# Kernel optimization log

Hardware: AMD Instinct MI355X
Metric: run time of the kernel (lower is better)

Reference implementation:

```python
import jax, jax.numpy as jnp
import numpy as np

N_NODES = 131072
N_EDGES = 1048576
N_GRAPHS = 1024
EMB = 96
HID = 64
OUT = 3
NEG_SLOPE = 0.2  # PyG GATConv default leaky_relu slope


def setup_inputs() -> dict:
    key = jax.random.key(0)
    ks = jax.random.split(key, 8)
    x = jax.random.normal(ks[0], (N_NODES, EMB), dtype=jnp.float32)
    edge_index = jax.random.randint(ks[1], (2, N_EDGES), 0, N_NODES, dtype=jnp.int64)
    batch = jnp.sort(jax.random.randint(ks[2], (N_NODES,), 0, N_GRAPHS, dtype=jnp.int64))
    s = 1.0 / np.sqrt(EMB)
    W = jax.random.uniform(ks[3], (EMB, HID), jnp.float32, -s, s)       # GATConv lin (no bias)
    att_src = jax.random.uniform(ks[4], (HID,), jnp.float32, -s, s)     # a_src
    att_dst = jax.random.uniform(ks[5], (HID,), jnp.float32, -s, s)     # a_dst
    bias_gat = jnp.zeros((HID,), jnp.float32)
    sf = 1.0 / np.sqrt(HID)
    fc_w = jax.random.uniform(ks[6], (OUT, HID), jnp.float32, -sf, sf)
    fc_b = jax.random.uniform(ks[7], (OUT,), jnp.float32, -sf, sf)
    return {"x": x, "edge_index": edge_index, "batch": batch, "W": W,
            "att_src": att_src, "att_dst": att_dst, "bias_gat": bias_gat,
            "fc_w": fc_w, "fc_b": fc_b}


def _segment_softmax(logits, seg, num_segments):
    # numerically stable softmax over edges grouped by target node
    m = jax.ops.segment_max(logits, seg, num_segments=num_segments)
    e = jnp.exp(logits - m[seg])
    z = jax.ops.segment_sum(e, seg, num_segments=num_segments)
    return e / (z[seg] + 1e-16)


def reference(x, edge_index, batch, W, att_src, att_dst, bias_gat, fc_w, fc_b):
    N = x.shape[0]
    # PyG GATConv (heads=1): add self loops
    loop = jnp.arange(N, dtype=edge_index.dtype)
    src = jnp.concatenate([edge_index[0], loop])
    dst = jnp.concatenate([edge_index[1], loop])

    h = x @ W                                    # [N, HID]
    a_s = h @ att_src                            # [N]
    a_d = h @ att_dst                            # [N]
    logits = jax.nn.leaky_relu(a_s[src] + a_d[dst], NEG_SLOPE)  # [E]
    alpha = _segment_softmax(logits, dst, N)     # softmax over in-edges per target
    out = jax.ops.segment_sum(alpha[:, None] * h[src], dst, num_segments=N)
    out = out + bias_gat                         # [N, HID]

    # global_mean_pool over graphs
    sums = jax.ops.segment_sum(out, batch, num_segments=N_GRAPHS)
    cnt = jax.ops.segment_sum(jnp.ones((N,), out.dtype), batch, num_segments=N_GRAPHS)
    pooled = sums / jnp.maximum(cnt, 1.0)[:, None]  # [G, HID]

    logits_out = pooled @ fc_w.T + fc_b          # [G, OUT]
    return jax.nn.log_softmax(logits_out, axis=1)
```

## Files before the change

### kernel.cpp

```cpp
#include <hip/hip_runtime.h>
#include <hip/hip_fp16.h>

#define N_NODES 131072
#define N_EDGES 1048576
#define N_GRAPHS 1024
#define EMB 96
#define HID 64
#define OUT 3
#define CAP 32
#define NBKT 512
#define NCHUNK 256
#define BCAP 32
#define LCAP 16

typedef _Float16 half8 __attribute__((ext_vector_type(8)));
typedef float float4v __attribute__((ext_vector_type(4)));

__global__ __launch_bounds__(512, 4) void k_front(
    const int* __restrict__ src, const int* __restrict__ dst,
    int* __restrict__ ebuf, int* __restrict__ ccnt,
    const float* __restrict__ x, const float* __restrict__ W,
    const float* __restrict__ att_src, const float* __restrict__ att_dst,
    __half* __restrict__ h, float* __restrict__ a_s, float* __restrict__ a_d,
    float* __restrict__ poolz)
{
    int tid = threadIdx.x;
    __shared__ int smem[NBKT * LCAP + NBKT];

    if (blockIdx.x < NCHUNK) {
        int blk = blockIdx.x;
        int* lists16 = smem;
        int* bcnt = smem + NBKT * LCAP;
        bcnt[tid] = 0;
        if (blk < 33) {
            int idx = blk * 512 + tid;
            if (idx < (N_GRAPHS * HID + N_GRAPHS) / 4)
                ((float4*)poolz)[idx] = (float4){0.f, 0.f, 0.f, 0.f};
        }
        __syncthreads();
        int e0 = blk * 4096;
        #pragma unroll
        for (int i = 0; i < 8; ++i) {
            int e = e0 + i * 512 + tid;
            int sv = src[e], dv = dst[e];
            int b = dv >> 8;
            int packed = (sv << 8) | (dv & 255);
            int r = atomicAdd(&bcnt[b], 1);
            if (r < LCAP)
                lists16[b * LCAP + r] = packed;
            else if (r < BCAP)
                ebuf[((size_t)blk * NBKT + b) * BCAP + r] = packed;
        }
        __syncthreads();
        #pragma unroll
        for (int it = 0; it < 16; ++it) {
            int idx = it * 512 + tid;
            int seg = idx >> 4, s = idx & 15;
            ebuf[((size_t)blk * NBKT + seg) * BCAP + s] = lists16[idx];
        }
        int v = bcnt[tid];
        ccnt[blk * NBKT + tid] = v < BCAP ? v : BCAP;
    } else {
        int sub = blockIdx.x - NCHUNK;
        _Float16* lwt = (_Float16*)smem;
        #pragma unroll
        for (int i = 0; i < 12; ++i) {
            int idx = i * 512 + tid;
            lwt[(idx & 63) * 104 + (idx >> 6)] = (_Float16)W[idx];
        }
        __syncthreads();

        int lane = tid & 63;
        int w = tid >> 6;
        int m16 = lane & 15;
        int quad = lane >> 4;
        int rowbase = sub * 128 + w * 16;

        half8 bf[4][3];
        #pragma unroll
        for (int nt = 0; nt < 4; ++nt)
            #pragma unroll
            for (int kb = 0; kb < 3; ++kb)
                bf[nt][kb] = *(const half8*)(lwt + (nt * 16 + m16) * 104
                                             + kb * 32 + quad * 8);

        float4v acc[4];
        #pragma unroll
        for (int nt = 0; nt < 4; ++nt)
            acc[nt] = (float4v){0.f, 0.f, 0.f, 0.f};

        const float* xrow = x + (size_t)(rowbase + m16) * EMB + quad * 8;
        #pragma unroll
        for (int kb = 0; kb < 3; ++kb) {
            float4 xa = *(const float4*)(xrow + kb * 32);
            float4 xb = *(const float4*)(xrow + kb * 32 + 4);
            half8 af;
            af[0] = (_Float16)xa.x; af[1] = (_Float16)xa.y;
            af[2] = (_Float16)xa.z; af[3] = (_Float16)xa.w;
            af[4] = (_Float16)xb.x; af[5] = (_Float16)xb.y;
            af[6] = (_Float16)xb.z; af[7] = (_Float16)xb.w;
            #pragma unroll
            for (int nt = 0; nt < 4; ++nt)
                acc[nt] = __builtin_amdgcn_mfma_f32_16x16x32_f16(
                    af, bf[nt][kb], acc[nt], 0, 0, 0);
        }

        float asv[4], adv[4];
        #pragma unroll
        for (int nt = 0; nt < 4; ++nt) {
            asv[nt] = att_src[nt * 16 + m16];
            adv[nt] = att_dst[nt * 16 + m16];
        }

        #pragma unroll
        for (int r = 0; r < 4; ++r) {
            int row = rowbase + quad * 4 + r;
            float ps = 0.f, pd = 0.f;
            #pragma unroll
            for (int nt = 0; nt < 4; ++nt) {
                float v = acc[nt][r];
                h[(size_t)row * HID + nt * 16 + m16] = __float2half(v);
                ps += v * asv[nt];
                pd += v * adv[nt];
            }
            #pragma unroll
            for (int off = 8; off >= 1; off >>= 1) {
                ps += __shfl_xor(ps, off, 64);
                pd += __shfl_xor(pd, off, 64);
            }
            if (m16 == 0) { a_s[row] = ps; a_d[row] = pd; }
        }
    }
}

__global__ __launch_bounds__(512, 2) void k_place_accum(
    const int* __restrict__ ebuf, const int* __restrict__ ccnt,
    const __half2* __restrict__ h2, const float* __restrict__ a_s,
    const float* __restrict__ a_d, const float* __restrict__ bias,
    __half2* __restrict__ out)
{
    int tid = threadIdx.x;
    int r_ = blockIdx.x & 15;
    int b = (blockIdx.x >> 4) * 8 + (r_ & 7);
    int half = r_ >> 3;
    __shared__ int lists[128 * CAP];
    __shared__ int cl[128];
    __shared__ int cm[NCHUNK];
    __shared__ float wbuf[32 * CAP];
    if (tid < 128) cl[tid] = 0;
    if (tid < NCHUNK) cm[tid] = ccnt[tid * NBKT + b];
    __syncthreads();

    int hbase = half << 7;

    {
        int e[8];
        #pragma unroll
        for (int k = 0; k < 8; ++k) {
            int c = k * 32 + (tid >> 4);
            e[k] = ebuf[((size_t)c * NBKT + b) * BCAP + (tid & 15)];
        }
        #pragma unroll
        for (int k = 0; k < 8; ++k) {
            int c = k * 32 + (tid >> 4);
            int local = e[k] & 255;
            if ((tid & 15) < cm[c] && (local >> 7) == half) {
                int slot = atomicAdd(&cl[local & 127], 1);
                if (slot < CAP)
                    lists[(local & 127) * CAP + slot] = e[k] >> 8;
            }
        }
    }
    if (tid < NCHUNK) {
        int n = cm[tid];
        for (int s = 16; s < n; ++s) {
            int ev = ebuf[((size_t)tid * NBKT + b) * BCAP + s];
            int local = ev & 255;
            if ((local >> 7) == half) {
                int slot = atomicAdd(&cl[local & 127], 1);
                if (slot < CAP)
                    lists[(local & 127) * CAP + slot] = ev >> 8;
            }
        }
    }
    __syncthreads();

    int lane = tid & 63;
    int sub = lane & 31;
    int gbase = lane & 32;
    int wv = tid >> 6;
    int grp = tid >> 5;
    float2 b2 = ((const float2*)bias)[sub];
    int nbase = b * 256 + hbase;

    for (int p = 0; p < 8; p += 2) {
        int localA = p * 16 + wv * 2 + (gbase >> 5);
        int localB = localA + 16;
        int nodeA = nbase + localA;
        int nodeB = nbase + localB;
        int degA = cl[localA]; if (degA > CAP) degA = CAP;
        int degB = cl[localB]; if (degB > CAP) degB = CAP;

        __half2 hvA = h2[(size_t)nodeA * 32 + sub];
        __half2 hvB = h2[(size_t)nodeB * 32 + sub];
        __half2 hgA[16], hgB[16];
        #pragma unroll
        for (int k = 0; k < 16; ++k) {
            int s = lists[localA * CAP + k];
            s = (k < degA) ? s : nodeA;
            hgA[k] = h2[(size_t)s * 32 + sub];
        }
        #pragma unroll
        for (int k = 0; k < 16; ++k) {
            int s = lists[localB * CAP + k];
            s = (k < degB) ? s : nodeB;
            hgB[k] = h2[(size_t)s * 32 + sub];
        }

        int svA = lists[localA * CAP + sub];
        int s_jA = (sub < degA) ? svA : nodeA;
        int svB = lists[localB * CAP + sub];
        int s_jB = (sub < degB) ? svB : nodeB;
        float asgA = a_s[s_jA];
        float asgB = a_s[s_jB];
        float adiA = a_d[nodeA], asiA = a_s[nodeA];
        float adiB = a_d[nodeB], asiB = a_s[nodeB];

        float tA = asgA + adiA; tA = tA > 0.f ? tA : 0.2f * tA;
        float w_jA = (sub < degA) ? __expf(tA) : 0.f;
        wbuf[grp * CAP + sub] = w_jA;
        float tB = asgB + adiB; tB = tB > 0.f ? tB : 0.2f * tB;
        float w_jB = (sub < degB) ? __expf(tB) : 0.f;
        wbuf[(16 + grp) * CAP + sub] = w_jB;

        float t0A = asiA + adiA; t0A = t0A > 0.f ? t0A : 0.2f * t0A;
        float w0A = __expf(t0A);
        float t0B = asiB + adiB; t0B = t0B > 0.f ? t0B : 0.2f * t0B;
        float w0B = __expf(t0B);

        float zA = w_jA, zB = w_jB;
        #pragma unroll
        for (int off = 16; off >= 1; off >>= 1) {
            zA += __shfl_xor(zA, off, 64);
            zB += __shfl_xor(zB, off, 64);
        }
        zA += w0A; zB += w0B;

        float2 accA, accB;
        accA.x = w0A * __half2float(hvA.x);
        accA.y = w0A * __half2float(hvA.y);
        accB.x = w0B * __half2float(hvB.x);
        accB.y = w0B * __half2float(hvB.y);
        #pragma unroll
        for (int k = 0; k < 16; ++k) {
            float wkA = wbuf[grp * CAP + k];
            accA.x += wkA * __half2float(hgA[k].x);
            accA.y += wkA * __half2float(hgA[k].y);
            float wkB = wbuf[(16 + grp) * CAP + k];
            accB.x += wkB * __half2float(hgB[k].x);
            accB.y += wkB * __half2float(hgB[k].y);
        }

        for (int j0 = 16; j0 < degA; j0 += 8) {
            __half2 g2[8];
            #pragma unroll
            for (int k = 0; k < 8; ++k) {
                int s = lists[localA * CAP + j0 + k];
                s = (j0 + k < degA) ? s : nodeA;
                g2[k] = h2[(size_t)s * 32 + sub];
            }
            #pragma unroll
            for (int k = 0; k < 8; ++k) {
                float wk = wbuf[grp * CAP + j0 + k];
                accA.x += wk * __half2float(g2[k].x);
                accA.y += wk * __half2float(g2[k].y);
            }
        }
        for (int j0 = 16; j0 < degB; j0 += 8) {
            __half2 g2[8];
            #pragma unroll
            for (int k = 0; k < 8; ++k) {
                int s = lists[localB * CAP + j0 + k];
                s = (j0 + k < degB) ? s : nodeB;
                g2[k] = h2[(size_t)s * 32 + sub];
            }
            #pragma unroll
            for (int k = 0; k < 8; ++k) {
                float wk = wbuf[(16 + grp) * CAP + j0 + k];
                accB.x += wk * __half2float(g2[k].x);
                accB.y += wk * __half2float(g2[k].y);
            }
        }

        float invA = 1.f / (zA + 1e-16f);
        float invB = 1.f / (zB + 1e-16f);
        out[(size_t)nodeA * 32 + sub] =
            __floats2half2_rn(accA.x * invA + b2.x, accA.y * invA + b2.y);
        out[(size_t)nodeB * 32 + sub] =
            __floats2half2_rn(accB.x * invB + b2.x, accB.y * invB + b2.y);
    }
}

__global__ __launch_bounds__(256) void k_pool(const __half* __restrict__ out,
    const int* __restrict__ batch, float* __restrict__ pool,
    float* __restrict__ gcnt)
{
    int lane = threadIdx.x & 63;
    int wv = blockIdx.x * 4 + (threadIdx.x >> 6);
    int base = wv * 64;
    int bv = batch[base + lane];
    int g_cur = __shfl(bv, 0);
    float acc = 0.f;
    int run = 0;
    for (int c = 0; c < 8; ++c) {
        int n0 = base + c * 8;
        float v[8];
        #pragma unroll
        for (int k = 0; k < 8; ++k)
            v[k] = __half2float(out[(size_t)(n0 + k) * HID + lane]);
        int b0 = __shfl(bv, c * 8);
        int b7 = __shfl(bv, c * 8 + 7);
        if (b0 == b7) {
            if (b0 != g_cur) {
                atomicAdd(&pool[g_cur * HID + lane], acc);
                if (lane == 0) atomicAdd(&gcnt[g_cur], (float)run);
                acc = 0.f; run = 0; g_cur = b0;
            }
            acc += ((v[0] + v[1]) + (v[2] + v[3]))
                 + ((v[4] + v[5]) + (v[6] + v[7]));
            run += 8;
        } else {
            #pragma unroll
            for (int k = 0; k < 8; ++k) {
                int g = __shfl(bv, c * 8 + k);
                if (g != g_cur) {
                    atomicAdd(&pool[g_cur * HID + lane], acc);
                    if (lane == 0) atomicAdd(&gcnt[g_cur], (float)run);
                    acc = 0.f; run = 0; g_cur = g;
                }
                acc += v[k]; ++run;
            }
        }
    }
    atomicAdd(&pool[g_cur * HID + lane], acc);
    if (lane == 0) atomicAdd(&gcnt[g_cur], (float)run);
}

__global__ __launch_bounds__(256) void k_head(const float* __restrict__ pool,
    const float* __restrict__ gcnt, const float* __restrict__ fc_w,
    const float* __restrict__ fc_b, float* __restrict__ out)
{
    int tid = threadIdx.x;
    int lane = tid & 63;
    int g = blockIdx.x * 4 + (tid >> 6);
    float p = pool[g * HID + lane] / fmaxf(gcnt[g], 1.0f);
    float l0 = p * fc_w[0 * HID + lane];
    float l1 = p * fc_w[1 * HID + lane];
    float l2 = p * fc_w[2 * HID + lane];
    #pragma unroll
    for (int off = 32; off >= 1; off >>= 1) {
        l0 += __shfl_xor(l0, off, 64);
        l1 += __shfl_xor(l1, off, 64);
        l2 += __shfl_xor(l2, off, 64);
    }
    l0 += fc_b[0]; l1 += fc_b[1]; l2 += fc_b[2];
    float m = fmaxf(l0, fmaxf(l1, l2));
    float lse = m + logf(__expf(l0 - m) + __expf(l1 - m) + __expf(l2 - m));
    if (lane == 0) {
        out[g * 3 + 0] = l0 - lse;
        out[g * 3 + 1] = l1 - lse;
        out[g * 3 + 2] = l2 - lse;
    }
}

extern "C" void kernel_launch(void* const* d_in, const int* in_sizes, int n_in,
                              void* d_out, int out_size, void* d_ws, size_t ws_size,
                              hipStream_t stream)
{
    const float* x        = (const float*)d_in[0];
    const int*   ei       = (const int*)d_in[1];
    const int*   batch    = (const int*)d_in[2];
    const float* W        = (const float*)d_in[3];
    const float* att_src  = (const float*)d_in[4];
    const float* att_dst  = (const float*)d_in[5];
    const float* bias_gat = (const float*)d_in[6];
    const float* fc_w     = (const float*)d_in[7];
    const float* fc_b     = (const float*)d_in[8];
    float* out = (float*)d_out;

    char* ws = (char*)d_ws;
    size_t off = 0;
    auto alloc = [&](size_t bytes) {
        void* p = ws + off;
        off += (bytes + 255) & ~(size_t)255;
        return p;
    };
    __half* h    = (__half*)alloc((size_t)N_NODES * HID * 2);
    float* pool  = (float*)alloc((size_t)N_GRAPHS * HID * 4);
    float* gcnt  = (float*)alloc((size_t)N_GRAPHS * 4);
    float* a_s   = (float*)alloc((size_t)N_NODES * 4);
    float* a_d   = (float*)alloc((size_t)N_NODES * 4);
    int*   ccnt  = (int*)  alloc((size_t)NCHUNK * NBKT * 4);
    int*   ebuf  = (int*)  alloc((size_t)NCHUNK * NBKT * BCAP * 4);
    __half* nout = (__half*)alloc((size_t)N_NODES * HID * 2);

    const int* e_src = ei;
    const int* e_dst = ei + N_EDGES;

    k_front<<<NCHUNK + 1024, 512, 0, stream>>>(e_src, e_dst, ebuf, ccnt,
                                               x, W, att_src, att_dst,
                                               h, a_s, a_d, pool);
    k_place_accum<<<NBKT * 2, 512, 0, stream>>>(ebuf, ccnt, (const __half2*)h,
                                                a_s, a_d, bias_gat,
                                                (__half2*)nout);
    k_pool <<<N_NODES / 256, 256, 0, stream>>>(nout, batch, pool, gcnt);
    k_head <<<N_GRAPHS / 4, 256, 0, stream>>>(pool, gcnt, fc_w, fc_b, out);
}
```

Baseline: 154.2 us.

## Fuse mean-pool accumulation into GAT aggregation kernel, drop node-output buffer

The separate pooling kernel is removed. Each wave keeps its 8 aggregated node results in registers, rounds them to half to match the old intermediate precision, and does a run-length segmented sum over the batch ids with atomics into the per-graph pool. This removes the write and re-read of the N×64 half output buffer and one kernel launch. In exchange there are more atomics, since each wave covers nodes strided by 16 and sorted runs are shorter, and register pressure rises from the extra result arrays.

```diff
diff --git a/kernel.cpp b/kernel.cpp
--- a/kernel.cpp
+++ b/kernel.cpp
@@ -137,7 +137,8 @@
     const int* __restrict__ ebuf, const int* __restrict__ ccnt,
     const __half2* __restrict__ h2, const float* __restrict__ a_s,
     const float* __restrict__ a_d, const float* __restrict__ bias,
-    __half2* __restrict__ out)
+    const int* __restrict__ batch, float* __restrict__ pool,
+    float* __restrict__ gcnt)
 {
     int tid = threadIdx.x;
     int r_ = blockIdx.x & 15;
@@ -193,7 +194,11 @@
     float2 b2 = ((const float2*)bias)[sub];
     int nbase = b * 256 + hbase;
 
+    float2 resA[4], resB[4];
+
+    #pragma unroll
     for (int p = 0; p < 8; p += 2) {
+        int it = p >> 1;
         int localA = p * 16 + wv * 2 + (gbase >> 5);
         int localB = localA + 16;
         int nodeA = nbase + localA;
@@ -294,56 +299,38 @@
 
         float invA = 1.f / (zA + 1e-16f);
         float invB = 1.f / (zB + 1e-16f);
-        out[(size_t)nodeA * 32 + sub] =
-            __floats2half2_rn(accA.x * invA + b2.x, accA.y * invA + b2.y);
-        out[(size_t)nodeB * 32 + sub] =
-            __floats2half2_rn(accB.x * invB + b2.x, accB.y * invB + b2.y);
-    }
-}
-
-__global__ __launch_bounds__(256) void k_pool(const __half* __restrict__ out,
-    const int* __restrict__ batch, float* __restrict__ pool,
-    float* __restrict__ gcnt)
-{
-    int lane = threadIdx.x & 63;
-    int wv = blockIdx.x * 4 + (threadIdx.x >> 6);
-    int base = wv * 64;
-    int bv = batch[base + lane];
-    int g_cur = __shfl(bv, 0);
-    float acc = 0.f;
-    int run = 0;
-    for (int c = 0; c < 8; ++c) {
-        int n0 = base + c * 8;
-        float v[8];
-        #pragma unroll
-        for (int k = 0; k < 8; ++k)
-            v[k] = __half2float(out[(size_t)(n0 + k) * HID + lane]);
-        int b0 = __shfl(bv, c * 8);
-        int b7 = __shfl(bv, c * 8 + 7);
-        if (b0 == b7) {
-            if (b0 != g_cur) {
-                atomicAdd(&pool[g_cur * HID + lane], acc);
-                if (lane == 0) atomicAdd(&gcnt[g_cur], (float)run);
-                acc = 0.f; run = 0; g_cur = b0;
-            }
-            acc += ((v[0] + v[1]) + (v[2] + v[3]))
-                 + ((v[4] + v[5]) + (v[6] + v[7]));
-            run += 8;
-        } else {
-            #pragma unroll
-            for (int k = 0; k < 8; ++k) {
-                int g = __shfl(bv, c * 8 + k);
-                if (g != g_cur) {
-                    atomicAdd(&pool[g_cur * HID + lane], acc);
-                    if (lane == 0) atomicAdd(&gcnt[g_cur], (float)run);
-                    acc = 0.f; run = 0; g_cur = g;
-                }
-                acc += v[k]; ++run;
-            }
-        }
-    }
-    atomicAdd(&pool[g_cur * HID + lane], acc);
-    if (lane == 0) atomicAdd(&gcnt[g_cur], (float)run);
+        resA[it].x = accA.x * invA + b2.x; resA[it].y = accA.y * invA + b2.y;
+        resB[it].x = accB.x * invB + b2.x; resB[it].y = accB.y * invB + b2.y;
+    }
+
+    {
+        int off = wv * 2 + (gbase >> 5);
+        float2 v[8];
+        #pragma unroll
+        for (int i = 0; i < 4; ++i) {
+            __half2 ha = __floats2half2_rn(resA[i].x, resA[i].y);
+            __half2 hb = __floats2half2_rn(resB[i].x, resB[i].y);
+            v[2 * i].x     = __half2float(ha.x); v[2 * i].y     = __half2float(ha.y);
+            v[2 * i + 1].x = __half2float(hb.x); v[2 * i + 1].y = __half2float(hb.y);
+        }
+        int g_cur = batch[nbase + off];
+        float2 racc = v[0];
+        float rcnt = 1.f;
+        #pragma unroll
+        for (int i = 1; i < 8; ++i) {
+            int g = batch[nbase + off + i * 16];
+            if (g != g_cur) {
+                atomicAdd(&pool[g_cur * HID + 2 * sub],     racc.x);
+                atomicAdd(&pool[g_cur * HID + 2 * sub + 1], racc.y);
+                if (sub == 0) atomicAdd(&gcnt[g_cur], rcnt);
+                g_cur = g; racc.x = 0.f; racc.y = 0.f; rcnt = 0.f;
+            }
+            racc.x += v[i].x; racc.y += v[i].y; rcnt += 1.f;
+        }
+        atomicAdd(&pool[g_cur * HID + 2 * sub],     racc.x);
+        atomicAdd(&pool[g_cur * HID + 2 * sub + 1], racc.y);
+        if (sub == 0) atomicAdd(&gcnt[g_cur], rcnt);
+    }
 }
 
 __global__ __launch_bounds__(256) void k_head(const float* __restrict__ pool,
@@ -402,7 +389,6 @@
     float* a_d   = (float*)alloc((size_t)N_NODES * 4);
     int*   ccnt  = (int*)  alloc((size_t)NCHUNK * NBKT * 4);
     int*   ebuf  = (int*)  alloc((size_t)NCHUNK * NBKT * BCAP * 4);
-    __half* nout = (__half*)alloc((size_t)N_NODES * HID * 2);
 
     const int* e_src = ei;
     const int* e_dst = ei + N_EDGES;
@@ -411,8 +397,7 @@
                                                x, W, att_src, att_dst,
                                                h, a_s, a_d, pool);
     k_place_accum<<<NBKT * 2, 512, 0, stream>>>(ebuf, ccnt, (const __half2*)h,
-                                                a_s, a_d, bias_gat,
-                                                (__half2*)nout);
-    k_pool <<<N_NODES / 256, 256, 0, stream>>>(nout, batch, pool, gcnt);
+                                                a_s, a_d, bias_gat, batch,
+                                                pool, gcnt);
     k_head <<<N_GRAPHS / 4, 256, 0, stream>>>(pool, gcnt, fc_w, fc_b, out);
 }
```

After: 190.4 us. 1.23x slower.
